# Kernel tuning notes

Hardware: AMD Instinct MI355X
Metric: run time of the kernel (lower is better)

## Reference

```python
import jax, jax.numpy as jnp
import numpy as np

TAU = 2.0      # LIFNode default tau
VTH = 1.0      # v_threshold
ALPHA = 2.0    # ATan surrogate alpha
EPS = 1e-5     # BatchNorm eps
SCALE = 0.125  # hardcoded attention scale
HEADS = 8

@jax.custom_vjp
def atan_spike(x):
    return (x >= 0.0).astype(x.dtype)

def _atan_fwd(x):
    return atan_spike(x), x

def _atan_bwd(x, g):
    sg = (ALPHA / 2.0) / (1.0 + (jnp.pi / 2.0 * ALPHA * x) ** 2)
    return (g * sg,)

atan_spike.defvjp(_atan_fwd, _atan_bwd)

def lif(x_seq):
    # multi-step LIF: v' = v + (x - v)/tau ; spike = H(v'-1) ; hard reset to 0 (detach_reset)
    def step(v, x):
        v = v + (x - v) / TAU
        s = atan_spike(v - VTH)
        v = v * (1.0 - jax.lax.stop_gradient(s))
        return v, s
    _, spikes = jax.lax.scan(step, jnp.zeros_like(x_seq[0]), x_seq)
    return spikes

def bn(x, gamma, beta, mean, var):
    # inference-mode BatchNorm1d over channel axis 2 of [T,B,C,N]
    inv = gamma / jnp.sqrt(var + EPS)
    return x * inv[None, None, :, None] + (beta - mean * inv)[None, None, :, None]

def setup_inputs() -> dict:
    key = jax.random.key(0)
    ks = jax.random.split(key, 24)
    T, B, C, H, W = 4, 8, 512, 32, 32
    inp = {"x": jax.random.normal(ks[0], (T, B, C, H, W), dtype=jnp.float32)}
    i = 1
    for p in ("q", "k", "v", "proj"):
        inp[p + "_w"] = jax.random.normal(ks[i], (C, C), dtype=jnp.float32) / np.sqrt(C); i += 1
        inp[p + "_gamma"] = jax.random.uniform(ks[i], (C,), minval=0.5, maxval=1.5, dtype=jnp.float32); i += 1
        inp[p + "_beta"] = 0.1 * jax.random.normal(ks[i], (C,), dtype=jnp.float32); i += 1
        inp[p + "_mean"] = 0.1 * jax.random.normal(ks[i], (C,), dtype=jnp.float32); i += 1
        inp[p + "_var"] = jax.random.uniform(ks[i], (C,), minval=0.5, maxval=1.5, dtype=jnp.float32); i += 1
    inp["proj_b"] = 0.1 * jax.random.normal(ks[i], (C,), dtype=jnp.float32)
    return inp

def reference(x, q_w, q_gamma, q_beta, q_mean, q_var,
              k_w, k_gamma, k_beta, k_mean, k_var,
              v_w, v_gamma, v_beta, v_mean, v_var,
              proj_w, proj_gamma, proj_beta, proj_mean, proj_var, proj_b):
    T, B, C, H, W = x.shape
    N = H * W
    d = C // HEADS
    s = lif(x).reshape(T, B, C, N)  # proj_lif then flatten HW

    def branch(w, g, b, m, v_):
        y = jnp.einsum('oc,tbcn->tbon', w, s)  # conv1x1 == channel GEMM
        y = lif(bn(y, g, b, m, v_))
        # [T,B,C,N] -> [T,B,h,N,d]
        return y.reshape(T, B, HEADS, d, N).transpose(0, 1, 2, 4, 3)

    q = branch(q_w, q_gamma, q_beta, q_mean, q_var)
    k = branch(k_w, k_gamma, k_beta, k_mean, k_var)
    v = branch(v_w, v_gamma, v_beta, v_mean, v_var)

    kv = jnp.einsum('tbhnd,tbhne->tbhde', k, v)          # k^T v : [T,B,h,d,d]
    att = jnp.einsum('tbhnd,tbhde->tbhne', q, kv) * SCALE  # [T,B,h,N,d]
    att = att.transpose(0, 1, 2, 4, 3).reshape(T, B, C, N)
    a = lif(att)

    y = jnp.einsum('oc,tbcn->tbon', proj_w, a) + proj_b[None, None, :, None]
    y = bn(y, proj_gamma, proj_beta, proj_mean, proj_var)
    return y.reshape(T, B, C, H, W)
```

## Files before the change

kernel.cpp:

```cpp
#include <hip/hip_runtime.h>
#include <cstdint>
#include <cstddef>

typedef unsigned short u16;
typedef __attribute__((ext_vector_type(8))) short sh8;
typedef __attribute__((ext_vector_type(8))) _Float16 hf8;
typedef __attribute__((ext_vector_type(4))) float f4;

#define MFMA16B(a, b, c) __builtin_amdgcn_mfma_f32_16x16x32_bf16((a), (b), (c), 0, 0, 0)
#define MFMA16H(a, b, c) __builtin_amdgcn_mfma_f32_16x16x32_f16((a), (b), (c), 0, 0, 0)

__device__ __forceinline__ u16 f2bf(float f) {
  union { float f; uint32_t u; } v; v.f = f;
  uint32_t u = v.u;
  uint32_t lsb = (u >> 16) & 1u;
  return (u16)((u + 0x7fffu + lsb) >> 16);
}
__device__ __forceinline__ float bf2f(u16 h) {
  union { uint32_t u; float f; } v; v.u = ((uint32_t)h) << 16;
  return v.f;
}

__device__ __forceinline__ void aload16(const void* g, void* l) {
  __builtin_amdgcn_global_load_lds(
      (const __attribute__((address_space(1))) uint32_t*)g,
      (__attribute__((address_space(3))) uint32_t*)l, 16, 0, 0);
}

__device__ __forceinline__ void pbar() {
  __builtin_amdgcn_sched_barrier(0);
  __builtin_amdgcn_s_barrier();
  __builtin_amdgcn_sched_barrier(0);
}
__device__ __forceinline__ void tile_bar() {
  asm volatile("s_waitcnt vmcnt(0)" ::: "memory");
  __builtin_amdgcn_s_barrier();
  __builtin_amdgcn_sched_barrier(0);
}

#define QUAD12(Af, Bf, MH, NH)                                                \
  {                                                                           \
    __builtin_amdgcn_s_setprio(1);                                            \
    _Pragma("unroll") for (int kk = 0; kk < 2; ++kk)                          \
      _Pragma("unroll") for (int nf = 0; nf < 2; ++nf)                        \
        _Pragma("unroll") for (int mf = 0; mf < 3; ++mf)                      \
          acc[(MH)*3 + mf][(NH)*2 + nf] = MFMA16H(                            \
              Af[mf][kk], Bf[nf][kk], acc[(MH)*3 + mf][(NH)*2 + nf]);         \
    __builtin_amdgcn_s_setprio(0);                                            \
  }

__global__ void prep_weights(const float* __restrict__ qw, const float* __restrict__ kw,
                             const float* __restrict__ vw, const float* __restrict__ pw,
                             u16* __restrict__ w2qkv, u16* __restrict__ w2p) {
  #pragma clang fp contract(off)
  int row = blockIdx.x;
  for (int c = threadIdx.x; c < 512; c += 256) {
    const float* src;
    if (row < 1536) {
      int br = row >> 9;
      src = (br == 0 ? qw : (br == 1 ? kw : vw)) + (size_t)(row & 511) * 512;
    } else {
      src = pw + (size_t)(row - 1536) * 512;
    }
    float w = src[c];
    _Float16 h0 = (_Float16)w;
    float r1 = w - (float)h0;
    _Float16 h1 = (_Float16)r1;
    union { _Float16 h; u16 u; } u0, u1;
    u0.h = h0; u1.h = h1;
    if (row < 1536) {
      w2qkv[(size_t)row * 1024 + c] = u0.u;
      w2qkv[(size_t)row * 1024 + 512 + c] = u1.u;
    } else {
      int m = row - 1536;
      w2p[(size_t)m * 512 + c] = u0.u;
      w2p[(size_t)(512 + m) * 512 + c] = u1.u;
    }
  }
}

__global__ void bn_prep(const float* __restrict__ g, const float* __restrict__ be,
                        const float* __restrict__ mu, const float* __restrict__ va,
                        float* __restrict__ inv, float* __restrict__ add) {
  #pragma clang fp contract(off)
  int i = blockIdx.x * 256 + threadIdx.x;
  if (i < 512) {
    float iv = g[i] / sqrtf(va[i] + 1e-5f);
    inv[i] = iv;
    add[i] = be[i] - mu[i] * iv;
  }
}

__global__ __launch_bounds__(256) void lif0(const float* __restrict__ x, u16* __restrict__ sT) {
  #pragma clang fp contract(off)
  __shared__ u16 st[64 * 80];
  const int tid = threadIdx.x;
  const int n0 = blockIdx.x * 64;
  const int c0 = blockIdx.y * 64;
  const int b = blockIdx.z;
  const int cl = tid >> 2;
  const int ns = (tid & 3) * 16;
  const int nr = tid >> 2;
  const int cs = (tid & 3) * 16;
  float vv[16];
#pragma unroll
  for (int i = 0; i < 16; i++) vv[i] = 0.f;
  for (int t = 0; t < 4; ++t) {
    const float* xp = x + ((size_t)((t * 8 + b) * 512 + c0 + cl)) * 1024 + n0 + ns;
#pragma unroll
    for (int q = 0; q < 4; ++q) {
      f4 xv = *(const f4*)(xp + q * 4);
#pragma unroll
      for (int j = 0; j < 4; ++j) {
        int i = q * 4 + j;
        float v2 = vv[i] + (xv[j] - vv[i]) * 0.5f;
        int spk = (v2 - 1.0f >= 0.0f);
        st[(ns + i) * 80 + cl] = spk ? (u16)0x3C00 : (u16)0;
        vv[i] = spk ? 0.0f : v2;
      }
    }
    __syncthreads();
    u16* gp = sT + ((size_t)((t * 8 + b) * 1024 + n0 + nr)) * 512 + c0 + cs;
    *(sh8*)(gp) = *(const sh8*)&st[nr * 80 + cs];
    *(sh8*)(gp + 8) = *(const sh8*)&st[nr * 80 + cs + 8];
    __syncthreads();
  }
}

__global__ __launch_bounds__(512, 2) void qkv_gemm(
    const u16* __restrict__ w2,
    const u16* __restrict__ sT,
    const float* __restrict__ inv4, const float* __restrict__ add4,
    u16* __restrict__ qs, u16* __restrict__ ks, u16* __restrict__ vs) {
  #pragma clang fp contract(off)
  __shared__ u16 lA[2][192 * 64];
  __shared__ u16 lB[2][256 * 64];
  const int tid = threadIdx.x;
  const int bid = blockIdx.x;
  const int orig = (bid & 7) * 32 + (bid >> 3);
  const int mI = orig & 7;
  const int nI = (orig >> 3) & 3;
  const int b  = orig >> 5;
  const int m0 = mI * 192;
  const int n0 = nI * 256;
  const int wid = tid >> 6, lane = tid & 63;
  const int l15 = lane & 15, l4 = lane >> 4;
  const int wm = wid >> 2, wn = wid & 3;
  const int srow = tid >> 3;
  const int sslot = (tid & 7) ^ (srow & 7);
  int aoff[3];
#pragma unroll
  for (int c = 0; c < 3; ++c)
    aoff[c] = (m0 + c * 64 + srow) * 1024 + sslot * 8;
  int boff[4];
#pragma unroll
  for (int c = 0; c < 4; ++c)
    boff[c] = (n0 + c * 64 + srow) * 512 + sslot * 8;

  auto stA = [&](int bf, int ii) {
    int k0 = (ii & 15) * 64;
#pragma unroll
    for (int c = 0; c < 3; ++c)
      aload16(w2 + (size_t)aoff[c] + k0, &lA[bf][c * 4096 + tid * 8]);
  };
  auto stB = [&](int bf, int ii, int c0) {
    int bk0 = (ii & 7) * 64;
    int tt = ii >> 4;
    const u16* bb = sT + (size_t)tt * 4194304 + (size_t)b * 524288;
#pragma unroll
    for (int c = c0; c < c0 + 2; ++c)
      aload16(bb + (size_t)boff[c] + bk0, &lB[bf][c * 4096 + tid * 8]);
  };

  const f4 fz = {0.f, 0.f, 0.f, 0.f};
  f4 acc[6][4];
  f4 vst[6][4];
#pragma unroll
  for (int i = 0; i < 6; i++)
#pragma unroll
    for (int j = 0; j < 4; j++) vst[i][j] = fz;

  stA(0, 0); stB(0, 0, 0); stB(0, 0, 2);
  tile_bar();
  int buf = 0;

  for (int t = 0; t < 4; ++t) {
#pragma unroll
    for (int i = 0; i < 6; i++)
#pragma unroll
      for (int j = 0; j < 4; j++) acc[i][j] = fz;

    for (int i = 0; i < 16; ++i) {
      const int ii = t * 16 + i;
      const bool pf = (ii < 63);
      hf8 A0[3][2], Bq[2][2];
#pragma unroll
      for (int mf = 0; mf < 3; ++mf)
#pragma unroll
        for (int kk = 0; kk < 2; ++kk) {
          int lr = wm * 96 + mf * 16 + l15;
          A0[mf][kk] = *(const hf8*)&lA[buf][lr * 64 + (((kk * 4 + l4) ^ (l15 & 7)) * 8)];
        }
#pragma unroll
      for (int nf = 0; nf < 2; ++nf)
#pragma unroll
        for (int kk = 0; kk < 2; ++kk) {
          int lr = wn * 64 + nf * 16 + l15;
          Bq[nf][kk] = *(const hf8*)&lB[buf][lr * 64 + (((kk * 4 + l4) ^ (l15 & 7)) * 8)];
        }
      if (pf) stA(buf ^ 1, ii + 1);
      pbar();
      QUAD12(A0, Bq, 0, 0);
      hf8 B1[2][2];
#pragma unroll
      for (int nf = 0; nf < 2; ++nf)
#pragma unroll
        for (int kk = 0; kk < 2; ++kk) {
          int lr = wn * 64 + (2 + nf) * 16 + l15;
          B1[nf][kk] = *(const hf8*)&lB[buf][lr * 64 + (((kk * 4 + l4) ^ (l15 & 7)) * 8)];
        }
      if (pf) stB(buf ^ 1, ii + 1, 0);
      pbar();
      QUAD12(A0, B1, 0, 1);
      hf8 A1[3][2];
#pragma unroll
      for (int mf = 0; mf < 3; ++mf)
#pragma unroll
        for (int kk = 0; kk < 2; ++kk) {
          int lr = wm * 96 + (3 + mf) * 16 + l15;
          A1[mf][kk] = *(const hf8*)&lA[buf][lr * 64 + (((kk * 4 + l4) ^ (l15 & 7)) * 8)];
        }
      if (pf) stB(buf ^ 1, ii + 1, 2);
      pbar();
      QUAD12(A1, B1, 1, 1);
#pragma unroll
      for (int nf = 0; nf < 2; ++nf)
#pragma unroll
        for (int kk = 0; kk < 2; ++kk) {
          int lr = wn * 64 + nf * 16 + l15;
          Bq[nf][kk] = *(const hf8*)&lB[buf][lr * 64 + (((kk * 4 + l4) ^ (l15 & 7)) * 8)];
        }
      pbar();
      QUAD12(A1, Bq, 1, 0);
      tile_bar();
      buf ^= 1;
    }
#pragma unroll
    for (int mf = 0; mf < 6; ++mf) {
      int f0 = m0 + wm * 96 + mf * 16;
      int br = f0 >> 9;
      u16* dst = br == 0 ? qs : (br == 1 ? ks : vs);
      int ocb = f0 & 511;
#pragma unroll
      for (int r = 0; r < 4; ++r) {
        int oc = ocb + l4 * 4 + r;
        float iv = inv4[br * 512 + oc];
        float ad = add4[br * 512 + oc];
        size_t rowbase = ((size_t)((t * 8 + b) * 512 + oc)) * 1024 + n0;
#pragma unroll
        for (int nf = 0; nf < 4; ++nf) {
          float z = acc[mf][nf][r] * iv + ad;
          float v2 = vst[mf][nf][r];
          v2 = v2 + (z - v2) * 0.5f;
          int spk = (v2 - 1.0f >= 0.0f);
          vst[mf][nf][r] = spk ? 0.0f : v2;
          dst[rowbase + wn * 64 + nf * 16 + l15] = spk ? (u16)0x3F80 : (u16)0;
        }
      }
    }
  }
}

__global__ __launch_bounds__(256) void kv_gemm(const u16* __restrict__ ks,
                                               const u16* __restrict__ vs,
                                               float* __restrict__ kvp) {
  const int tbh = blockIdx.x;
  const int tid = threadIdx.x;
  const int wv = tid >> 6, lane = tid & 63, l15 = lane & 15, l4 = lane >> 4;
  const size_t cb = ((size_t)(tbh >> 3) * 512 + (size_t)(tbh & 7) * 64) * 1024;
  const u16* vbase = vs + cb;
  const u16* kbase = ks + cb;
  const f4 fz = {0.f, 0.f, 0.f, 0.f};
  f4 acc[4];
#pragma unroll
  for (int i = 0; i < 4; i++) acc[i] = fz;
  for (int s = 0; s < 32; ++s) {
    int kk = s * 32 + l4 * 8;
    sh8 av = *(const sh8*)(vbase + (size_t)(wv * 16 + l15) * 1024 + kk);
#pragma unroll
    for (int df = 0; df < 4; ++df) {
      sh8 bk = *(const sh8*)(kbase + (size_t)(df * 16 + l15) * 1024 + kk);
      acc[df] = MFMA16B(av, bk, acc[df]);
    }
  }
  float* out = kvp + (size_t)tbh * 4096;
#pragma unroll
  for (int df = 0; df < 4; ++df)
#pragma unroll
    for (int r = 0; r < 4; ++r)
      out[(wv * 16 + l4 * 4 + r) * 64 + df * 16 + l15] = acc[df][r];
}

__global__ __launch_bounds__(256) void att_lif(const u16* __restrict__ qs,
                                               const float* __restrict__ kvp,
                                               u16* __restrict__ aT) {
  #pragma clang fp contract(off)
  __shared__ u16 ldsb[64 * 72 * 2 + 128 * 72];
  u16* lkhi = ldsb;
  u16* lklo = ldsb + 64 * 72;
  u16* lqT = ldsb + 64 * 72 * 2;
  u16* lsp = ldsb;
  const int tid = threadIdx.x;
  const int n0 = blockIdx.x * 128;
  const int b = blockIdx.y >> 3;
  const int h = blockIdx.y & 7;
  const int wv = tid >> 6, lane = tid & 63, l15 = lane & 15, l4 = lane >> 4;
  const int e_s = tid >> 2, ds_ = (tid & 3) * 16;
  const f4 fz = {0.f, 0.f, 0.f, 0.f};
  f4 vst[4][2];
#pragma unroll
  for (int i = 0; i < 4; i++)
#pragma unroll
    for (int j = 0; j < 2; j++) vst[i][j] = fz;

  for (int t = 0; t < 4; ++t) {
    int tb = t * 8 + b;
    int tbh = tb * 8 + h;
    {
      const float* base = kvp + (size_t)tbh * 4096 + e_s * 64 + ds_;
#pragma unroll
      for (int q = 0; q < 4; ++q) {
        f4 s4 = *(const f4*)(base + q * 4);
#pragma unroll
        for (int j = 0; j < 4; ++j) {
          float sv = s4[j];
          u16 hb = f2bf(sv);
          float lof = sv - bf2f(hb);
          lkhi[e_s * 72 + ds_ + q * 4 + j] = hb;
          lklo[e_s * 72 + ds_ + q * 4 + j] = f2bf(lof);
        }
      }
    }
    {
      const u16* qb = qs + ((size_t)tb * 512 + h * 64) * 1024 + n0;
#pragma unroll
      for (int it = 0; it < 4; ++it) {
        int lin = it * 2048 + tid * 8;
        int d = lin >> 7, j0 = lin & 127;
        sh8 qv = *(const sh8*)(qb + (size_t)d * 1024 + j0);
#pragma unroll
        for (int j = 0; j < 8; ++j) lqT[(j0 + j) * 72 + d] = (u16)qv[j];
      }
    }
    __syncthreads();
    f4 acc[4][2];
#pragma unroll
    for (int i = 0; i < 4; i++)
#pragma unroll
      for (int j = 0; j < 2; j++) acc[i][j] = fz;
#pragma unroll
    for (int ksx = 0; ksx < 2; ++ksx) {
      sh8 bq[2];
#pragma unroll
      for (int nf = 0; nf < 2; ++nf)
        bq[nf] = *(const sh8*)&lqT[(wv * 32 + nf * 16 + l15) * 72 + ksx * 32 + l4 * 8];
#pragma unroll
      for (int mf = 0; mf < 4; ++mf) {
        sh8 ah = *(const sh8*)&lkhi[(mf * 16 + l15) * 72 + ksx * 32 + l4 * 8];
        sh8 al = *(const sh8*)&lklo[(mf * 16 + l15) * 72 + ksx * 32 + l4 * 8];
#pragma unroll
        for (int nf = 0; nf < 2; ++nf) {
          acc[mf][nf] = MFMA16B(ah, bq[nf], acc[mf][nf]);
          acc[mf][nf] = MFMA16B(al, bq[nf], acc[mf][nf]);
        }
      }
    }
    __syncthreads();
#pragma unroll
    for (int mf = 0; mf < 4; ++mf)
#pragma unroll
      for (int nf = 0; nf < 2; ++nf)
#pragma unroll
        for (int r = 0; r < 4; ++r) {
          float xatt = acc[mf][nf][r] * 0.125f;
          float v2 = vst[mf][nf][r];
          v2 = v2 + (xatt - v2) * 0.5f;
          int spk = (v2 - 1.0f >= 0.0f);
          vst[mf][nf][r] = spk ? 0.0f : v2;
          int e = mf * 16 + l4 * 4 + r;
          int n = wv * 32 + nf * 16 + l15;
          lsp[n * 72 + e] = spk ? (u16)0x3C00 : (u16)0;
        }
    __syncthreads();
    {
#pragma unroll
      for (int it = 0; it < 2; ++it) {
        int lin = it * 256 + tid;
        int n = lin >> 2, es = (lin & 3) * 16;
        u16* gp = aT + ((size_t)(tb * 1024 + n0 + n)) * 512 + h * 64 + es;
        *(sh8*)gp = *(const sh8*)&lsp[n * 72 + es];
        *(sh8*)(gp + 8) = *(const sh8*)&lsp[n * 72 + es + 8];
      }
    }
    __syncthreads();
  }
}

__global__ __launch_bounds__(256, 2) void proj_gemm(
    const u16* __restrict__ w2, const u16* __restrict__ aT,
    const float* __restrict__ inv4, const float* __restrict__ add4,
    const float* __restrict__ pb, float* __restrict__ out) {
  #pragma clang fp contract(off)
  __shared__ u16 lA[2 * 128 * 32];
  __shared__ u16 lB[128 * 32];
  const int tid = threadIdx.x;
  const int m0 = blockIdx.x * 128;
  const int n0 = blockIdx.y * 128;
  const int tb = blockIdx.z;
  const int lane = tid & 63, wv = tid >> 6;
  const int l15 = lane & 15, l4 = lane >> 4;
  const int wm = wv >> 1, wn = wv & 1;
  const int rA = tid >> 2;
  const int kswz = (((tid & 3) ^ ((tid >> 3) & 3)) * 8);
  const int sA = (l4 ^ ((l15 >> 1) & 3)) * 8;

  size_t aoff[4];
#pragma unroll
  for (int c = 0; c < 4; ++c) {
    int rf = c * 64 + rA;
    int sp = rf >> 7, r = rf & 127;
    aoff[c] = (size_t)(sp * 512 + m0 + r) * 512 + kswz;
  }
  size_t boff[2];
#pragma unroll
  for (int c = 0; c < 2; ++c) boff[c] = (size_t)(c * 64 + rA) * 512 + kswz;

  const f4 fz = {0.f, 0.f, 0.f, 0.f};
  f4 acc[4][4];
#pragma unroll
  for (int i = 0; i < 4; i++)
#pragma unroll
    for (int j = 0; j < 4; j++) acc[i][j] = fz;
  const u16* aTt = aT + ((size_t)tb * 1024 + n0) * 512;

  for (int k0 = 0; k0 < 512; k0 += 32) {
#pragma unroll
    for (int c = 0; c < 4; ++c)
      aload16(w2 + aoff[c] + k0, &lA[c * 2048 + tid * 8]);
#pragma unroll
    for (int c = 0; c < 2; ++c)
      aload16(aTt + boff[c] + k0, &lB[c * 2048 + tid * 8]);
    __syncthreads();
    hf8 bfr[4];
#pragma unroll
    for (int nf = 0; nf < 4; ++nf)
      bfr[nf] = *(const hf8*)&lB[(wn * 64 + nf * 16 + l15) * 32 + sA];
#pragma unroll
    for (int sp = 0; sp < 2; ++sp) {
#pragma unroll
      for (int mf = 0; mf < 4; ++mf) {
        hf8 afr = *(const hf8*)&lA[sp * 4096 + (wm * 64 + mf * 16 + l15) * 32 + sA];
#pragma unroll
        for (int nf = 0; nf < 4; ++nf) acc[mf][nf] = MFMA16H(afr, bfr[nf], acc[mf][nf]);
      }
    }
    __syncthreads();
  }
#pragma unroll
  for (int mf = 0; mf < 4; ++mf) {
#pragma unroll
    for (int r = 0; r < 4; ++r) {
      int o = m0 + wm * 64 + mf * 16 + l4 * 4 + r;
      float iv = inv4[3 * 512 + o];
      float ad = add4[3 * 512 + o];
      float bias = pb[o];
      size_t rowbase = ((size_t)(tb * 512 + o)) * 1024 + n0;
#pragma unroll
      for (int nf = 0; nf < 4; ++nf) {
        float z = (acc[mf][nf][r] + bias) * iv + ad;
        out[rowbase + wn * 64 + nf * 16 + l15] = z;
      }
    }
  }
}

extern "C" void kernel_launch(void* const* d_in, const int* in_sizes, int n_in,
                              void* d_out, int out_size, void* d_ws, size_t ws_size,
                              hipStream_t stream) {
  const float* x = (const float*)d_in[0];
  const float* qw = (const float*)d_in[1];
  const float* kw = (const float*)d_in[6];
  const float* vw = (const float*)d_in[11];
  const float* pw = (const float*)d_in[16];
  const float* pb = (const float*)d_in[21];

  char* p = (char*)d_ws;
  u16* w2qkv = (u16*)p; p += (size_t)1536 * 1024 * 2;
  u16* w2p = (u16*)p;   p += (size_t)2 * 512 * 512 * 2;
  float* inv4 = (float*)p; p += 4 * 512 * 4;
  float* add4 = (float*)p; p += 4 * 512 * 4;
  u16* sT = (u16*)p;    p += (size_t)4 * 8 * 1024 * 512 * 2;
  u16* qs = (u16*)p;    p += (size_t)4 * 8 * 512 * 1024 * 2;
  u16* ks = (u16*)p;    p += (size_t)4 * 8 * 512 * 1024 * 2;
  u16* vs = (u16*)p;    p += (size_t)4 * 8 * 512 * 1024 * 2;
  float* kvp = (float*)p; p += (size_t)256 * 4096 * 4;
  u16* aT = sT;
  float* out = (float*)d_out;

  prep_weights<<<dim3(2048), dim3(256), 0, stream>>>(qw, kw, vw, pw, w2qkv, w2p);
  for (int s = 0; s < 4; ++s) {
    const float* g  = (const float*)d_in[2 + s * 5];
    const float* be = (const float*)d_in[3 + s * 5];
    const float* mu = (const float*)d_in[4 + s * 5];
    const float* va = (const float*)d_in[5 + s * 5];
    bn_prep<<<dim3(2), dim3(256), 0, stream>>>(g, be, mu, va, inv4 + s * 512, add4 + s * 512);
  }
  lif0<<<dim3(16, 8, 8), dim3(256), 0, stream>>>(x, sT);
  qkv_gemm<<<dim3(256), dim3(512), 0, stream>>>(w2qkv, sT, inv4, add4, qs, ks, vs);
  kv_gemm<<<dim3(256), dim3(256), 0, stream>>>(ks, vs, kvp);
  att_lif<<<dim3(8, 64), dim3(256), 0, stream>>>(qs, kvp, aT);
  proj_gemm<<<dim3(4, 8, 32), dim3(256), 0, stream>>>(w2p, aT, inv4, add4, pb, out);
}
```

Measured before the change: 251.6 us.

## Triple-buffer B tiles in QKV GEMM with two-ahead prefetch and partial waitcnt

Turns the B (spike activation) LDS staging in the QKV GEMM into a three-stage ring, prefetching tile ii+2 while A stays double-buffered. Each iteration now waits only until the newest 4 loads are outstanding (vmcnt(4)) rather than draining all loads. The goal is to hide global-load latency behind more MFMA work. In exchange LDS use rises by 32KB per block, which may limit the two-blocks-per-CU occupancy. The vmcnt-based ordering must also stay correct against the A loads issued in the same iteration.

```diff
diff --git a/kernel.cpp b/kernel.cpp
--- a/kernel.cpp
+++ b/kernel.cpp
@@ -29,11 +29,6 @@
 
 __device__ __forceinline__ void pbar() {
   __builtin_amdgcn_sched_barrier(0);
-  __builtin_amdgcn_s_barrier();
-  __builtin_amdgcn_sched_barrier(0);
-}
-__device__ __forceinline__ void tile_bar() {
-  asm volatile("s_waitcnt vmcnt(0)" ::: "memory");
   __builtin_amdgcn_s_barrier();
   __builtin_amdgcn_sched_barrier(0);
 }
@@ -134,7 +129,7 @@
     u16* __restrict__ qs, u16* __restrict__ ks, u16* __restrict__ vs) {
   #pragma clang fp contract(off)
   __shared__ u16 lA[2][192 * 64];
-  __shared__ u16 lB[2][256 * 64];
+  __shared__ u16 lB[3][256 * 64];
   const int tid = threadIdx.x;
   const int bid = blockIdx.x;
   const int orig = (bid & 7) * 32 + (bid >> 3);
@@ -157,19 +152,21 @@
   for (int c = 0; c < 4; ++c)
     boff[c] = (n0 + c * 64 + srow) * 512 + sslot * 8;
 
-  auto stA = [&](int bf, int ii) {
-    int k0 = (ii & 15) * 64;
+  auto stA = [&](int ii2) {
+    int k0 = (ii2 & 15) * 64;
+    u16* d = &lA[ii2 & 1][0];
 #pragma unroll
     for (int c = 0; c < 3; ++c)
-      aload16(w2 + (size_t)aoff[c] + k0, &lA[bf][c * 4096 + tid * 8]);
+      aload16(w2 + (size_t)aoff[c] + k0, d + c * 4096 + tid * 8);
   };
-  auto stB = [&](int bf, int ii, int c0) {
-    int bk0 = (ii & 7) * 64;
-    int tt = ii >> 4;
+  auto stB = [&](int ii2) {
+    int bk0 = (ii2 & 7) * 64;
+    int tt = ii2 >> 4;
     const u16* bb = sT + (size_t)tt * 4194304 + (size_t)b * 524288;
-#pragma unroll
-    for (int c = c0; c < c0 + 2; ++c)
-      aload16(bb + (size_t)boff[c] + bk0, &lB[bf][c * 4096 + tid * 8]);
+    u16* d = &lB[ii2 % 3][0];
+#pragma unroll
+    for (int c = 0; c < 4; ++c)
+      aload16(bb + (size_t)boff[c] + bk0, d + c * 4096 + tid * 8);
   };
 
   const f4 fz = {0.f, 0.f, 0.f, 0.f};
@@ -180,9 +177,10 @@
 #pragma unroll
     for (int j = 0; j < 4; j++) vst[i][j] = fz;
 
-  stA(0, 0); stB(0, 0, 0); stB(0, 0, 2);
-  tile_bar();
-  int buf = 0;
+  stA(0); stB(0); stB(1);
+  asm volatile("s_waitcnt vmcnt(4)" ::: "memory");
+  __builtin_amdgcn_s_barrier();
+  __builtin_amdgcn_sched_barrier(0);
 
   for (int t = 0; t < 4; ++t) {
 #pragma unroll
@@ -192,23 +190,25 @@
 
     for (int i = 0; i < 16; ++i) {
       const int ii = t * 16 + i;
-      const bool pf = (ii < 63);
+      const u16* bufA = &lA[ii & 1][0];
+      const u16* bufB = &lB[ii % 3][0];
       hf8 A0[3][2], Bq[2][2];
 #pragma unroll
       for (int mf = 0; mf < 3; ++mf)
 #pragma unroll
         for (int kk = 0; kk < 2; ++kk) {
           int lr = wm * 96 + mf * 16 + l15;
-          A0[mf][kk] = *(const hf8*)&lA[buf][lr * 64 + (((kk * 4 + l4) ^ (l15 & 7)) * 8)];
+          A0[mf][kk] = *(const hf8*)&bufA[lr * 64 + (((kk * 4 + l4) ^ (l15 & 7)) * 8)];
         }
 #pragma unroll
       for (int nf = 0; nf < 2; ++nf)
 #pragma unroll
         for (int kk = 0; kk < 2; ++kk) {
           int lr = wn * 64 + nf * 16 + l15;
-          Bq[nf][kk] = *(const hf8*)&lB[buf][lr * 64 + (((kk * 4 + l4) ^ (l15 & 7)) * 8)];
-        }
-      if (pf) stA(buf ^ 1, ii + 1);
+          Bq[nf][kk] = *(const hf8*)&bufB[lr * 64 + (((kk * 4 + l4) ^ (l15 & 7)) * 8)];
+        }
+      if (ii < 63) stA(ii + 1);
+      if (ii < 62) stB(ii + 2);
       pbar();
       QUAD12(A0, Bq, 0, 0);
       hf8 B1[2][2];
@@ -217,9 +217,8 @@
 #pragma unroll
         for (int kk = 0; kk < 2; ++kk) {
           int lr = wn * 64 + (2 + nf) * 16 + l15;
-          B1[nf][kk] = *(const hf8*)&lB[buf][lr * 64 + (((kk * 4 + l4) ^ (l15 & 7)) * 8)];
-        }
-      if (pf) stB(buf ^ 1, ii + 1, 0);
+          B1[nf][kk] = *(const hf8*)&bufB[lr * 64 + (((kk * 4 + l4) ^ (l15 & 7)) * 8)];
+        }
       pbar();
       QUAD12(A0, B1, 0, 1);
       hf8 A1[3][2];
@@ -228,9 +227,8 @@
 #pragma unroll
         for (int kk = 0; kk < 2; ++kk) {
           int lr = wm * 96 + (3 + mf) * 16 + l15;
-          A1[mf][kk] = *(const hf8*)&lA[buf][lr * 64 + (((kk * 4 + l4) ^ (l15 & 7)) * 8)];
-        }
-      if (pf) stB(buf ^ 1, ii + 1, 2);
+          A1[mf][kk] = *(const hf8*)&bufA[lr * 64 + (((kk * 4 + l4) ^ (l15 & 7)) * 8)];
+        }
       pbar();
       QUAD12(A1, B1, 1, 1);
 #pragma unroll
@@ -238,12 +236,17 @@
 #pragma unroll
         for (int kk = 0; kk < 2; ++kk) {
           int lr = wn * 64 + nf * 16 + l15;
-          Bq[nf][kk] = *(const hf8*)&lB[buf][lr * 64 + (((kk * 4 + l4) ^ (l15 & 7)) * 8)];
+          Bq[nf][kk] = *(const hf8*)&bufB[lr * 64 + (((kk * 4 + l4) ^ (l15 & 7)) * 8)];
         }
       pbar();
       QUAD12(A1, Bq, 1, 0);
-      tile_bar();
-      buf ^= 1;
+      if (ii < 62) {
+        asm volatile("s_waitcnt vmcnt(4)" ::: "memory");
+      } else {
+        asm volatile("s_waitcnt vmcnt(0)" ::: "memory");
+      }
+      __builtin_amdgcn_s_barrier();
+      __builtin_amdgcn_sched_barrier(0);
     }
 #pragma unroll
     for (int mf = 0; mf < 6; ++mf) {
```

Measured after the change: 256.4 us. About the same (+1.9%).
